# Kernel tuning notes

Hardware: AMD Instinct MI355X
Metric: run time of the kernel (lower is better)

## Reference

```python
import jax, jax.numpy as jnp
import numpy as np
import math

THETA = 10000.0

def apply_rope(x, start_pos=0):
    # x: [B, H, S, D], rotate-half RoPE
    B, H, S, D = x.shape
    pos = jnp.arange(start_pos, start_pos + S, dtype=jnp.float32)
    inv_freq = 1.0 / (THETA ** (jnp.arange(0, D, 2, dtype=jnp.float32) / D))  # [D/2]
    ang = pos[:, None] * inv_freq[None, :]  # [S, D/2]
    cos, sin = jnp.cos(ang), jnp.sin(ang)
    x1, x2 = jnp.split(x, 2, axis=-1)
    return jnp.concatenate([x1 * cos - x2 * sin, x1 * sin + x2 * cos], axis=-1)


def setup_inputs() -> dict:
    key = jax.random.key(0)
    ks = jax.random.split(key, 9)
    B, S, E, H, D = 2, 2048, 2048, 16, 128
    s = 0.02
    return {
        "x": jax.random.normal(ks[0], (B, S, E), jnp.float32),
        "W_q": jax.random.normal(ks[1], (E, H * D), jnp.float32) * s,
        "b_q": jnp.zeros((H * D,), jnp.float32),
        "W_k": jax.random.normal(ks[2], (E, D), jnp.float32) * s,
        "b_k": jnp.zeros((D,), jnp.float32),
        "W_v": jax.random.normal(ks[3], (E, D), jnp.float32) * s,
        "b_v": jnp.zeros((D,), jnp.float32),
        "W_o": jax.random.normal(ks[4], (H * D, E), jnp.float32) * s,
        "b_o": jnp.zeros((E,), jnp.float32),
    }


def reference(x, W_q, b_q, W_k, b_k, W_v, b_v, W_o, b_o):
    B, S, E = x.shape
    D = W_k.shape[1]
    H = W_q.shape[1] // D
    # projections (weights stored [in, out])
    q = (x @ W_q + b_q).reshape(B, S, H, D).transpose(0, 2, 1, 3)   # [B,H,S,D]
    k = (x @ W_k + b_k).reshape(B, S, 1, D).transpose(0, 2, 1, 3)   # [B,1,S,D]
    v = (x @ W_v + b_v).reshape(B, S, 1, D).transpose(0, 2, 1, 3)   # [B,1,S,D]
    # RoPE (cache is None -> start_pos = 0)
    q = apply_rope(q, 0)
    k = apply_rope(k, 0)
    # shared-KV attention: k head dim broadcasts over H q heads
    scores = jnp.einsum("bhqd,bokd->bhqk", q, k) / math.sqrt(D)     # [B,H,S,S]
    causal = jnp.tril(jnp.ones((S, S), dtype=bool))
    scores = jnp.where(causal, scores, -jnp.inf)
    attn = jax.nn.softmax(scores, axis=-1)
    out = jnp.einsum("bhqk,bokd->bhqd", attn, v)                    # [B,H,S,D]
    out = out.transpose(0, 2, 1, 3).reshape(B, S, H * D)
    out = out @ W_o + b_o                                           # dropout is identity in eval
    return out
```

## Files before the change

### kernel.cpp

```cpp
#include <hip/hip_runtime.h>
#include <stdint.h>

typedef __bf16 bf16x8 __attribute__((ext_vector_type(8)));
typedef __bf16 bf16x2 __attribute__((ext_vector_type(2)));
typedef float  f32x4  __attribute__((ext_vector_type(4)));
typedef short  s16x8  __attribute__((ext_vector_type(8)));

__device__ inline unsigned short f2b(float f) {
  unsigned int u = __builtin_bit_cast(unsigned int, f);
  u += 0x7FFFu + ((u >> 16) & 1u);
  return (unsigned short)(u >> 16);
}
__device__ inline float b2f(unsigned short h) {
  unsigned int u = ((unsigned int)h) << 16;
  return __builtin_bit_cast(float, u);
}
__device__ inline unsigned int pkcvt(float a, float b) {
  bf16x2 t;
  t[0] = (__bf16)a;
  t[1] = (__bf16)b;
  return __builtin_bit_cast(unsigned int, t);
}
__device__ inline void gload_lds16(const void* g, void* l) {
  __builtin_amdgcn_global_load_lds(
      (const __attribute__((address_space(1))) unsigned int*)g,
      (__attribute__((address_space(3))) unsigned int*)l, 16, 0, 0);
}

__global__ void k_cvt_bf16(const float* __restrict__ in, unsigned short* __restrict__ out, int n4) {
  int i = blockIdx.x * blockDim.x + threadIdx.x;
  if (i < n4) {
    float4 v = ((const float4*)in)[i];
    ushort4 o;
    o.x = f2b(v.x); o.y = f2b(v.y); o.z = f2b(v.z); o.w = f2b(v.w);
    ((ushort4*)out)[i] = o;
  }
}

__global__ void k_transpose(const float* __restrict__ Wq, const float* __restrict__ Wk,
                            const float* __restrict__ Wv, const float* __restrict__ Wo,
                            unsigned short* __restrict__ dstQKV, unsigned short* __restrict__ dstO) {
  __shared__ float tile[32][33];
  int n0 = blockIdx.x * 32;
  int k0 = blockIdx.y * 32;
  const float* src; int ldn, noff, K;
  unsigned short* dst;
  if (blockIdx.z == 0) {
    K = 2048; dst = dstQKV;
    if (n0 < 2048)       { src = Wq; ldn = 2048; noff = n0; }
    else if (n0 < 2176)  { src = Wk; ldn = 128;  noff = n0 - 2048; }
    else                 { src = Wv; ldn = 128;  noff = n0 - 2176; }
  } else {
    if (n0 >= 2048) return;
    K = 2048; dst = dstO;
    src = Wo; ldn = 2048; noff = n0;
  }
  int tx = threadIdx.x & 31, ty = threadIdx.x >> 5;
  for (int yy = ty; yy < 32; yy += 8)
    tile[yy][tx] = src[(size_t)(k0 + yy) * ldn + noff + tx];
  __syncthreads();
  for (int yy = ty; yy < 32; yy += 8)
    dst[(size_t)(n0 + yy) * K + k0 + tx] = f2b(tile[tx][yy]);
}

__global__ void k_bias_concat(const float* __restrict__ bq, const float* __restrict__ bk,
                              const float* __restrict__ bv, float* __restrict__ dst) {
  int i = blockIdx.x * 256 + threadIdx.x;
  if (i < 2304) dst[i] = (i < 2048) ? bq[i] : (i < 2176 ? bk[i - 2048] : bv[i - 2176]);
}

template<int OUT_BF16>
__global__ __launch_bounds__(256)
void k_gemm_lds(const unsigned short* __restrict__ A, const unsigned short* __restrict__ Bt,
                const float* __restrict__ bias, void* __restrict__ Cout,
                int M, int N, int K) {
  __shared__ unsigned short As[2][4096];
  __shared__ unsigned short Bs[2][4096];
  const int tid  = threadIdx.x;
  const int lane = tid & 63, wid = tid >> 6;
  const int lr = lane & 15, lk = lane >> 4;
  const int wr = wid >> 1,  wc = wid & 1;
  const int mb = blockIdx.y * 128, nb = blockIdx.x * 128;

  const int srow = tid >> 2, scb = (tid & 3) * 8;
  const size_t gA = (size_t)(mb + srow) * K + scb;
  const size_t gB = (size_t)(nb + srow) * K + scb;
  const int ldso = wid * 512;

  f32x4 acc[4][4];
  #pragma unroll
  for (int i = 0; i < 4; ++i)
    #pragma unroll
    for (int j = 0; j < 4; ++j) acc[i][j] = (f32x4){0.f, 0.f, 0.f, 0.f};

  auto stage = [&](int buf, int kt) {
    const size_t ko = (size_t)kt * 32;
    gload_lds16(A  + gA + ko,                  &As[buf][ldso]);
    gload_lds16(A  + gA + 64 * (size_t)K + ko, &As[buf][2048 + ldso]);
    gload_lds16(Bt + gB + ko,                  &Bs[buf][ldso]);
    gload_lds16(Bt + gB + 64 * (size_t)K + ko, &Bs[buf][2048 + ldso]);
  };

  const int ktn = K >> 5;
  stage(0, 0);

  int cur = 0;
  #pragma unroll 1
  for (int kt = 0; kt < ktn; ++kt) {
    if (kt + 1 < ktn) {
      stage(cur ^ 1, kt + 1);
      asm volatile("s_waitcnt vmcnt(4)" ::: "memory");
    } else {
      asm volatile("s_waitcnt vmcnt(0)" ::: "memory");
    }
    __builtin_amdgcn_sched_barrier(0);
    __builtin_amdgcn_s_barrier();
    bf16x8 af[4], bfv[4];
    #pragma unroll
    for (int m = 0; m < 4; ++m)
      af[m]  = *(const bf16x8*)&As[cur][(wr * 64 + m * 16 + lr) * 32 + lk * 8];
    #pragma unroll
    for (int n = 0; n < 4; ++n)
      bfv[n] = *(const bf16x8*)&Bs[cur][(wc * 64 + n * 16 + lr) * 32 + lk * 8];
    #pragma unroll
    for (int m = 0; m < 4; ++m)
      #pragma unroll
      for (int n = 0; n < 4; ++n)
        acc[m][n] = __builtin_amdgcn_mfma_f32_16x16x32_bf16(af[m], bfv[n], acc[m][n], 0, 0, 0);
    __builtin_amdgcn_s_barrier();
    cur ^= 1;
  }

  const int r0 = mb + wr * 64, c0 = nb + wc * 64;
  #pragma unroll
  for (int m = 0; m < 4; ++m) {
    #pragma unroll
    for (int n = 0; n < 4; ++n) {
      int col = c0 + n * 16 + lr;
      float bb = bias[col];
      #pragma unroll
      for (int r = 0; r < 4; ++r) {
        int row = r0 + m * 16 + lk * 4 + r;
        float v = acc[m][n][r] + bb;
        if (OUT_BF16) ((unsigned short*)Cout)[(size_t)row * N + col] = f2b(v);
        else          ((float*)Cout)[(size_t)row * N + col] = v;
      }
    }
  }
}

__global__ void k_rope(const unsigned short* __restrict__ qkv,
                       unsigned short* __restrict__ qr,
                       unsigned short* __restrict__ kr,
                       int S, int H) {
  int R = blockIdx.x * 4 + (threadIdx.x >> 6);
  int lane = threadIdx.x & 63;
  int per_b = S * (H + 1);
  int b = R / per_b;
  int rem = R - b * per_b;
  int s = rem / (H + 1);
  int j = rem - s * (H + 1);
  const unsigned short* src = qkv + (size_t)(b * S + s) * 2304 + (j < H ? j * 128 : 2048);
  float x1 = b2f(src[lane]);
  float x2 = b2f(src[lane + 64]);
  float invf = expf(-(float)lane * (9.210340371976184f / 64.0f));
  float ang = (float)s * invf;
  float c = cosf(ang), sn = sinf(ang);
  float o1 = x1 * c - x2 * sn;
  float o2 = x1 * sn + x2 * c;
  unsigned short* dst;
  if (j < H) {
    const float scale = 0.08838834764831845f;
    o1 *= scale; o2 *= scale;
    dst = qr + ((size_t)(b * H + j) * S + s) * 128;
  } else {
    dst = kr + ((size_t)(b * S) + s) * 128;
  }
  dst[lane]      = f2b(o1);
  dst[lane + 64] = f2b(o2);
}

__global__ void k_vtrans(const unsigned short* __restrict__ qkv,
                         unsigned short* __restrict__ vt, int S) {
  __shared__ unsigned short tile[32][33];
  int b = blockIdx.z;
  int s0 = blockIdx.x * 32, d0 = blockIdx.y * 32;
  int tx = threadIdx.x & 31, ty = threadIdx.x >> 5;
  for (int yy = ty; yy < 32; yy += 8)
    tile[yy][tx] = qkv[(size_t)(b * S + s0 + yy) * 2304 + 2176 + d0 + tx];
  __syncthreads();
  for (int yy = ty; yy < 32; yy += 8)
    vt[((size_t)b * 128 + d0 + yy) * S + s0 + tx] = tile[tx][yy];
}

__global__ __launch_bounds__(512, 4)
void k_attn(const unsigned short* __restrict__ qr,
            const unsigned short* __restrict__ kr,
            const unsigned short* __restrict__ vt,
            unsigned short* __restrict__ attn_out,
            int S, int H) {
  const int b = blockIdx.z;
  const int nqt = gridDim.x;
  const int qt = blockIdx.z ? (int)blockIdx.x : (nqt - 1 - (int)blockIdx.x);
  const int qb0 = qt * 64;
  const int tid = threadIdx.x, wid = tid >> 6, lane = tid & 63;
  const int lr = lane & 15, lk = lane >> 4;
  const int hh = wid >> 2, w4 = wid & 3;
  const int h = blockIdx.y * 2 + hh;
  const int qw = qb0 + w4 * 16;

  __shared__ unsigned short Kt[2][64 * 128];
  __shared__ unsigned short Vt[2][128 * 64];

  const char* kbyte = (const char*)(kr + (size_t)b * S * 128);
  const char* vbyte = (const char*)(vt + (size_t)b * 128 * S);
  const size_t vrow_bytes = (size_t)S * 2;

  const unsigned short* qptr = qr + ((size_t)(b * H + h) * S + (qw + lr)) * 128;
  bf16x8 aq[4];
  #pragma unroll
  for (int kk = 0; kk < 4; ++kk) aq[kk] = *(const bf16x8*)(qptr + kk * 32 + lk * 8);

  f32x4 accO[8];
  #pragma unroll
  for (int t = 0; t < 8; ++t) accO[t] = (f32x4){0.f, 0.f, 0.f, 0.f};
  float lsum = 0.f;

  const int vsw = ((lr & 3) | ((lr >> 1) & 4)) << 4;

  auto stage = [&](int buf, int kb) {
    const char* kg = kbyte + (size_t)kb * 256;
    #pragma unroll
    for (int r = 0; r < 2; ++r) {
      int row = (tid >> 4) + r * 32;
      int sw = ((row & 3) | ((row >> 1) & 4)) << 4;
      const char* src = kg + row * 256 + (((tid & 15) << 4) ^ sw);
      gload_lds16(src, (void*)((char*)&Kt[buf][0] + (wid * 4 + r * 32) * 256));
    }
    const char* vg = vbyte + (size_t)kb * 2;
    #pragma unroll
    for (int r = 0; r < 2; ++r) {
      int d = (tid >> 3) + r * 64;
      int sw = ((d & 3) | ((d >> 1) & 4)) << 4;
      const char* src = vg + (size_t)d * vrow_bytes + (((tid & 7) << 4) ^ sw);
      gload_lds16(src, (void*)((char*)&Vt[buf][0] + (wid * 8 + r * 64) * 128));
    }
  };

  int cur = 0;
  stage(0, 0);

  #pragma unroll 1
  for (int kb = 0; kb <= qb0; kb += 64) {
    if (kb + 64 <= qb0) {
      stage(cur ^ 1, kb + 64);
      asm volatile("s_waitcnt vmcnt(4)" ::: "memory");
    } else {
      asm volatile("s_waitcnt vmcnt(0)" ::: "memory");
    }
    __builtin_amdgcn_sched_barrier(0);
    __builtin_amdgcn_s_barrier();
    const bool diag = (kb == qb0);
    const unsigned short* Kc = &Kt[cur][0];
    const unsigned short* Vc = &Vt[cur][0];

    bf16x8 kf[4][4];
    #pragma unroll
    for (int m = 0; m < 4; ++m) {
      const int row = ((m >> 1) << 5) + ((m & 1) << 2) + ((lr >> 2) << 3) + (lr & 3);
      const int sw = ((row & 3) | ((row >> 1) & 4)) << 4;
      const char* kl = (const char*)Kc + row * 256;
      #pragma unroll
      for (int kk = 0; kk < 4; ++kk)
        kf[m][kk] = *(const bf16x8*)(kl + ((kk * 64 + lk * 16) ^ sw));
    }
    f32x4 s4[4];
    #pragma unroll
    for (int m = 0; m < 4; ++m) s4[m] = (f32x4){0.f, 0.f, 0.f, 0.f};
    __builtin_amdgcn_s_setprio(1);
    #pragma unroll
    for (int kk = 0; kk < 4; ++kk)
      #pragma unroll
      for (int m = 0; m < 4; ++m)
        s4[m] = __builtin_amdgcn_mfma_f32_16x16x32_bf16(kf[m][kk], aq[kk], s4[m], 0, 0, 0);
    __builtin_amdgcn_s_setprio(0);

    uint2 pk[4];
    #pragma unroll
    for (int m = 0; m < 4; ++m) {
      const int kbase = ((m >> 1) << 5) + ((m & 1) << 2) + lk * 8;
      float p[4];
      #pragma unroll
      for (int r = 0; r < 4; ++r) {
        float v = __expf(s4[m][r]);
        if (diag && (kbase + r) > (w4 * 16 + lr)) v = 0.f;
        p[r] = v;
        lsum += v;
      }
      pk[m].x = pkcvt(p[0], p[1]);
      pk[m].y = pkcvt(p[2], p[3]);
    }
    uint4 ua, ub;
    ua.x = pk[0].x; ua.y = pk[0].y; ua.z = pk[1].x; ua.w = pk[1].y;
    ub.x = pk[2].x; ub.y = pk[2].y; ub.z = pk[3].x; ub.w = pk[3].y;
    bf16x8 pa0 = __builtin_bit_cast(bf16x8, ua);
    bf16x8 pa1 = __builtin_bit_cast(bf16x8, ub);

    __builtin_amdgcn_s_setprio(1);
    #pragma unroll
    for (int t = 0; t < 8; ++t) {
      const char* vl = (const char*)(Vc + (t * 16 + lr) * 64);
      bf16x8 bv0 = *(const bf16x8*)(vl + ((lk * 16) ^ vsw));
      accO[t] = __builtin_amdgcn_mfma_f32_16x16x32_bf16(pa0, bv0, accO[t], 0, 0, 0);
      bf16x8 bv1 = *(const bf16x8*)(vl + ((64 + lk * 16) ^ vsw));
      accO[t] = __builtin_amdgcn_mfma_f32_16x16x32_bf16(pa1, bv1, accO[t], 0, 0, 0);
    }
    __builtin_amdgcn_s_setprio(0);
    __builtin_amdgcn_s_barrier();
    cur ^= 1;
  }

  lsum += __shfl_xor(lsum, 16);
  lsum += __shfl_xor(lsum, 32);
  float rl[4];
  #pragma unroll
  for (int r = 0; r < 4; ++r) rl[r] = 1.0f / __shfl(lsum, lk * 4 + r);
  #pragma unroll
  for (int t = 0; t < 8; ++t) {
    #pragma unroll
    for (int r = 0; r < 4; ++r) {
      int srow = qw + lk * 4 + r;
      float o = accO[t][r] * rl[r];
      attn_out[((size_t)(b * S) + srow) * 2048 + h * 128 + t * 16 + lr] = f2b(o);
    }
  }
}

extern "C" void kernel_launch(void* const* d_in, const int* in_sizes, int n_in,
                              void* d_out, int out_size, void* d_ws, size_t ws_size,
                              hipStream_t stream) {
  const float* x  = (const float*)d_in[0];
  const float* Wq = (const float*)d_in[1];
  const float* bq = (const float*)d_in[2];
  const float* Wk = (const float*)d_in[3];
  const float* bk = (const float*)d_in[4];
  const float* Wv = (const float*)d_in[5];
  const float* bv = (const float*)d_in[6];
  const float* Wo = (const float*)d_in[7];
  const float* bo = (const float*)d_in[8];

  const int B = 2, S = 2048, E = 2048, H = 16, D = 128;
  const int M = B * S;
  const int Nqkv = H * D + 2 * D;

  char* w = (char*)d_ws;
  unsigned short* xb    = (unsigned short*)w;
  unsigned short* WqkvT = (unsigned short*)(w + 16777216);
  unsigned short* qkv   = (unsigned short*)(w + 16777216 + 9437184);
  unsigned short* qr    = (unsigned short*)(w + 16777216 + 9437184 + 18874368);
  unsigned short* kr    = qr + (size_t)B * H * S * D;
  unsigned short* vtb   = kr + (size_t)B * S * D;
  float*          cbias = (float*)(vtb + (size_t)B * S * D);
  unsigned short* WoT   = (unsigned short*)(cbias + 4096);
  unsigned short* attn_out = xb;

  k_cvt_bf16<<<dim3((M * E / 4) / 256), 256, 0, stream>>>(x, xb, M * E / 4);
  k_transpose<<<dim3(Nqkv / 32, E / 32, 2), 256, 0, stream>>>(Wq, Wk, Wv, Wo, WqkvT, WoT);
  k_bias_concat<<<dim3(9), 256, 0, stream>>>(bq, bk, bv, cbias);
  k_gemm_lds<1><<<dim3(Nqkv / 128, M / 128), 256, 0, stream>>>(xb, WqkvT, cbias, (void*)qkv, M, Nqkv, E);
  k_rope<<<dim3(B * S * (H + 1) / 4), 256, 0, stream>>>(qkv, qr, kr, S, H);
  k_vtrans<<<dim3(S / 32, D / 32, B), 256, 0, stream>>>(qkv, vtb, S);
  k_attn<<<dim3(S / 64, H / 2, B), 512, 0, stream>>>(qr, kr, vtb, attn_out, S, H);
  k_gemm_lds<0><<<dim3(E / 128, M / 128), 256, 0, stream>>>(attn_out, WoT, bo, (void*)d_out, M, E, H * D);
}
```

Measured before the change: 214.5 us.

## Restructure attention to one head per block with two query groups per wave

Each attention block now covers a single head and a 128-row query tile with 4 waves, and each wave handles 32 query rows as two 16-row groups. Every K/V fragment read from LDS therefore feeds twice as many MFMAs, which halves LDS traffic per unit of compute. Waves whose rows end before the current KV tile skip it, and the per-batch alternating tile order is replaced by uniform reverse ordering. In exchange each wave holds more accumulator registers and occupancy drops (launch bounds 256,2), and the causal workload per block is less balanced.

```diff
diff --git a/kernel.cpp b/kernel.cpp
--- a/kernel.cpp
+++ b/kernel.cpp
@@ -193,21 +193,18 @@
     vt[((size_t)b * 128 + d0 + yy) * S + s0 + tx] = tile[tx][yy];
 }
 
-__global__ __launch_bounds__(512, 4)
+__global__ __launch_bounds__(256, 2)
 void k_attn(const unsigned short* __restrict__ qr,
             const unsigned short* __restrict__ kr,
             const unsigned short* __restrict__ vt,
             unsigned short* __restrict__ attn_out,
             int S, int H) {
-  const int b = blockIdx.z;
-  const int nqt = gridDim.x;
-  const int qt = blockIdx.z ? (int)blockIdx.x : (nqt - 1 - (int)blockIdx.x);
-  const int qb0 = qt * 64;
+  const int b = blockIdx.z, h = blockIdx.y;
+  const int qt = gridDim.x - 1 - blockIdx.x;
+  const int qb0 = qt * 128;
   const int tid = threadIdx.x, wid = tid >> 6, lane = tid & 63;
   const int lr = lane & 15, lk = lane >> 4;
-  const int hh = wid >> 2, w4 = wid & 3;
-  const int h = blockIdx.y * 2 + hh;
-  const int qw = qb0 + w4 * 16;
+  const int qw = qb0 + wid * 32;
 
   __shared__ unsigned short Kt[2][64 * 128];
   __shared__ unsigned short Vt[2][128 * 64];
@@ -216,122 +213,149 @@
   const char* vbyte = (const char*)(vt + (size_t)b * 128 * S);
   const size_t vrow_bytes = (size_t)S * 2;
 
-  const unsigned short* qptr = qr + ((size_t)(b * H + h) * S + (qw + lr)) * 128;
-  bf16x8 aq[4];
-  #pragma unroll
-  for (int kk = 0; kk < 4; ++kk) aq[kk] = *(const bf16x8*)(qptr + kk * 32 + lk * 8);
-
-  f32x4 accO[8];
-  #pragma unroll
-  for (int t = 0; t < 8; ++t) accO[t] = (f32x4){0.f, 0.f, 0.f, 0.f};
-  float lsum = 0.f;
+  bf16x8 aq[2][4];
+  #pragma unroll
+  for (int g = 0; g < 2; ++g) {
+    const unsigned short* qptr = qr + ((size_t)(b * H + h) * S + (qw + g * 16 + lr)) * 128;
+    #pragma unroll
+    for (int kk = 0; kk < 4; ++kk) aq[g][kk] = *(const bf16x8*)(qptr + kk * 32 + lk * 8);
+  }
+
+  f32x4 accO[2][8];
+  #pragma unroll
+  for (int g = 0; g < 2; ++g)
+    #pragma unroll
+    for (int t = 0; t < 8; ++t) accO[g][t] = (f32x4){0.f, 0.f, 0.f, 0.f};
+  float lsum[2] = {0.f, 0.f};
 
   const int vsw = ((lr & 3) | ((lr >> 1) & 4)) << 4;
+  int krow_[4], ksw_[4];
+  #pragma unroll
+  for (int m = 0; m < 4; ++m) {
+    int row = ((m >> 1) << 5) + ((m & 1) << 2) + ((lr >> 2) << 3) + (lr & 3);
+    krow_[m] = row;
+    ksw_[m] = ((row & 3) | ((row >> 1) & 4)) << 4;
+  }
 
   auto stage = [&](int buf, int kb) {
     const char* kg = kbyte + (size_t)kb * 256;
     #pragma unroll
-    for (int r = 0; r < 2; ++r) {
-      int row = (tid >> 4) + r * 32;
+    for (int r = 0; r < 4; ++r) {
+      int row = (tid >> 4) + r * 16;
       int sw = ((row & 3) | ((row >> 1) & 4)) << 4;
       const char* src = kg + row * 256 + (((tid & 15) << 4) ^ sw);
-      gload_lds16(src, (void*)((char*)&Kt[buf][0] + (wid * 4 + r * 32) * 256));
+      gload_lds16(src, (void*)((char*)&Kt[buf][0] + r * 4096 + wid * 1024));
     }
     const char* vg = vbyte + (size_t)kb * 2;
     #pragma unroll
-    for (int r = 0; r < 2; ++r) {
-      int d = (tid >> 3) + r * 64;
+    for (int r = 0; r < 4; ++r) {
+      int d = (tid >> 3) + r * 32;
       int sw = ((d & 3) | ((d >> 1) & 4)) << 4;
       const char* src = vg + (size_t)d * vrow_bytes + (((tid & 7) << 4) ^ sw);
-      gload_lds16(src, (void*)((char*)&Vt[buf][0] + (wid * 8 + r * 64) * 128));
+      gload_lds16(src, (void*)((char*)&Vt[buf][0] + r * 4096 + wid * 1024));
     }
   };
 
+  const int nkv = (qb0 + 128) >> 6;
+  stage(0, 0);
   int cur = 0;
-  stage(0, 0);
 
   #pragma unroll 1
-  for (int kb = 0; kb <= qb0; kb += 64) {
-    if (kb + 64 <= qb0) {
-      stage(cur ^ 1, kb + 64);
-      asm volatile("s_waitcnt vmcnt(4)" ::: "memory");
+  for (int it = 0; it < nkv; ++it) {
+    const int kb = it << 6;
+    if (it + 1 < nkv) {
+      stage(cur ^ 1, (it + 1) << 6);
+      asm volatile("s_waitcnt vmcnt(8)" ::: "memory");
     } else {
       asm volatile("s_waitcnt vmcnt(0)" ::: "memory");
     }
     __builtin_amdgcn_sched_barrier(0);
     __builtin_amdgcn_s_barrier();
-    const bool diag = (kb == qb0);
-    const unsigned short* Kc = &Kt[cur][0];
-    const unsigned short* Vc = &Vt[cur][0];
-
-    bf16x8 kf[4][4];
-    #pragma unroll
-    for (int m = 0; m < 4; ++m) {
-      const int row = ((m >> 1) << 5) + ((m & 1) << 2) + ((lr >> 2) << 3) + (lr & 3);
-      const int sw = ((row & 3) | ((row >> 1) & 4)) << 4;
-      const char* kl = (const char*)Kc + row * 256;
-      #pragma unroll
-      for (int kk = 0; kk < 4; ++kk)
-        kf[m][kk] = *(const bf16x8*)(kl + ((kk * 64 + lk * 16) ^ sw));
-    }
-    f32x4 s4[4];
-    #pragma unroll
-    for (int m = 0; m < 4; ++m) s4[m] = (f32x4){0.f, 0.f, 0.f, 0.f};
-    __builtin_amdgcn_s_setprio(1);
-    #pragma unroll
-    for (int kk = 0; kk < 4; ++kk)
-      #pragma unroll
-      for (int m = 0; m < 4; ++m)
-        s4[m] = __builtin_amdgcn_mfma_f32_16x16x32_bf16(kf[m][kk], aq[kk], s4[m], 0, 0, 0);
-    __builtin_amdgcn_s_setprio(0);
-
-    uint2 pk[4];
-    #pragma unroll
-    for (int m = 0; m < 4; ++m) {
-      const int kbase = ((m >> 1) << 5) + ((m & 1) << 2) + lk * 8;
-      float p[4];
-      #pragma unroll
-      for (int r = 0; r < 4; ++r) {
-        float v = __expf(s4[m][r]);
-        if (diag && (kbase + r) > (w4 * 16 + lr)) v = 0.f;
-        p[r] = v;
-        lsum += v;
-      }
-      pk[m].x = pkcvt(p[0], p[1]);
-      pk[m].y = pkcvt(p[2], p[3]);
-    }
-    uint4 ua, ub;
-    ua.x = pk[0].x; ua.y = pk[0].y; ua.z = pk[1].x; ua.w = pk[1].y;
-    ub.x = pk[2].x; ub.y = pk[2].y; ub.z = pk[3].x; ub.w = pk[3].y;
-    bf16x8 pa0 = __builtin_bit_cast(bf16x8, ua);
-    bf16x8 pa1 = __builtin_bit_cast(bf16x8, ub);
-
-    __builtin_amdgcn_s_setprio(1);
-    #pragma unroll
-    for (int t = 0; t < 8; ++t) {
-      const char* vl = (const char*)(Vc + (t * 16 + lr) * 64);
-      bf16x8 bv0 = *(const bf16x8*)(vl + ((lk * 16) ^ vsw));
-      accO[t] = __builtin_amdgcn_mfma_f32_16x16x32_bf16(pa0, bv0, accO[t], 0, 0, 0);
-      bf16x8 bv1 = *(const bf16x8*)(vl + ((64 + lk * 16) ^ vsw));
-      accO[t] = __builtin_amdgcn_mfma_f32_16x16x32_bf16(pa1, bv1, accO[t], 0, 0, 0);
-    }
-    __builtin_amdgcn_s_setprio(0);
+
+    if (kb <= qw + 31) {
+      const unsigned short* Kc = &Kt[cur][0];
+      const unsigned short* Vc = &Vt[cur][0];
+
+      f32x4 s4[2][4];
+      #pragma unroll
+      for (int g = 0; g < 2; ++g)
+        #pragma unroll
+        for (int m = 0; m < 4; ++m) s4[g][m] = (f32x4){0.f, 0.f, 0.f, 0.f};
+      __builtin_amdgcn_s_setprio(1);
+      #pragma unroll
+      for (int kk = 0; kk < 4; ++kk) {
+        bf16x8 kfk[4];
+        #pragma unroll
+        for (int m = 0; m < 4; ++m)
+          kfk[m] = *(const bf16x8*)((const char*)Kc + krow_[m] * 256 + ((kk * 64 + lk * 16) ^ ksw_[m]));
+        #pragma unroll
+        for (int m = 0; m < 4; ++m) {
+          s4[0][m] = __builtin_amdgcn_mfma_f32_16x16x32_bf16(kfk[m], aq[0][kk], s4[0][m], 0, 0, 0);
+          s4[1][m] = __builtin_amdgcn_mfma_f32_16x16x32_bf16(kfk[m], aq[1][kk], s4[1][m], 0, 0, 0);
+        }
+      }
+      __builtin_amdgcn_s_setprio(0);
+
+      bf16x8 pa[2][2];
+      #pragma unroll
+      for (int g = 0; g < 2; ++g) {
+        const int rowq = qw + g * 16 + lr;
+        const bool domask = (kb + 64) > (qw + g * 16);
+        uint2 pk[4];
+        #pragma unroll
+        for (int m = 0; m < 4; ++m) {
+          const int kb_m = kb + ((m >> 1) << 5) + ((m & 1) << 2) + lk * 8;
+          float p[4];
+          #pragma unroll
+          for (int r = 0; r < 4; ++r) {
+            float v = __expf(s4[g][m][r]);
+            if (domask && (kb_m + r) > rowq) v = 0.f;
+            p[r] = v;
+            lsum[g] += v;
+          }
+          pk[m].x = pkcvt(p[0], p[1]);
+          pk[m].y = pkcvt(p[2], p[3]);
+        }
+        uint4 ua, ub;
+        ua.x = pk[0].x; ua.y = pk[0].y; ua.z = pk[1].x; ua.w = pk[1].y;
+        ub.x = pk[2].x; ub.y = pk[2].y; ub.z = pk[3].x; ub.w = pk[3].y;
+        pa[g][0] = __builtin_bit_cast(bf16x8, ua);
+        pa[g][1] = __builtin_bit_cast(bf16x8, ub);
+      }
+
+      __builtin_amdgcn_s_setprio(1);
+      #pragma unroll
+      for (int t = 0; t < 8; ++t) {
+        const char* vl = (const char*)(Vc + (t * 16 + lr) * 64);
+        bf16x8 bv0 = *(const bf16x8*)(vl + ((lk * 16) ^ vsw));
+        bf16x8 bv1 = *(const bf16x8*)(vl + ((64 + lk * 16) ^ vsw));
+        accO[0][t] = __builtin_amdgcn_mfma_f32_16x16x32_bf16(pa[0][0], bv0, accO[0][t], 0, 0, 0);
+        accO[1][t] = __builtin_amdgcn_mfma_f32_16x16x32_bf16(pa[1][0], bv0, accO[1][t], 0, 0, 0);
+        accO[0][t] = __builtin_amdgcn_mfma_f32_16x16x32_bf16(pa[0][1], bv1, accO[0][t], 0, 0, 0);
+        accO[1][t] = __builtin_amdgcn_mfma_f32_16x16x32_bf16(pa[1][1], bv1, accO[1][t], 0, 0, 0);
+      }
+      __builtin_amdgcn_s_setprio(0);
+    }
     __builtin_amdgcn_s_barrier();
     cur ^= 1;
   }
 
-  lsum += __shfl_xor(lsum, 16);
-  lsum += __shfl_xor(lsum, 32);
-  float rl[4];
-  #pragma unroll
-  for (int r = 0; r < 4; ++r) rl[r] = 1.0f / __shfl(lsum, lk * 4 + r);
-  #pragma unroll
-  for (int t = 0; t < 8; ++t) {
-    #pragma unroll
-    for (int r = 0; r < 4; ++r) {
-      int srow = qw + lk * 4 + r;
-      float o = accO[t][r] * rl[r];
-      attn_out[((size_t)(b * S) + srow) * 2048 + h * 128 + t * 16 + lr] = f2b(o);
+  #pragma unroll
+  for (int g = 0; g < 2; ++g) {
+    float ls = lsum[g];
+    ls += __shfl_xor(ls, 16);
+    ls += __shfl_xor(ls, 32);
+    float rl[4];
+    #pragma unroll
+    for (int r = 0; r < 4; ++r) rl[r] = 1.0f / __shfl(ls, lk * 4 + r);
+    #pragma unroll
+    for (int t = 0; t < 8; ++t) {
+      #pragma unroll
+      for (int r = 0; r < 4; ++r) {
+        int srow = qw + g * 16 + lk * 4 + r;
+        float o = accO[g][t][r] * rl[r];
+        attn_out[((size_t)(b * S) + srow) * 2048 + h * 128 + t * 16 + lr] = f2b(o);
+      }
     }
   }
 }
@@ -370,6 +394,6 @@
   k_gemm_lds<1><<<dim3(Nqkv / 128, M / 128), 256, 0, stream>>>(xb, WqkvT, cbias, (void*)qkv, M, Nqkv, E);
   k_rope<<<dim3(B * S * (H + 1) / 4), 256, 0, stream>>>(qkv, qr, kr, S, H);
   k_vtrans<<<dim3(S / 32, D / 32, B), 256, 0, stream>>>(qkv, vtb, S);
-  k_attn<<<dim3(S / 64, H / 2, B), 512, 0, stream>>>(qr, kr, vtb, attn_out, S, H);
+  k_attn<<<dim3(S / 128, H, B), 256, 0, stream>>>(qr, kr, vtb, attn_out, S, H);
   k_gemm_lds<0><<<dim3(E / 128, M / 128), 256, 0, stream>>>(attn_out, WoT, bo, (void*)d_out, M, E, H * D);
 }
```

New measurement: 223.2 us. +4.1%, slower.
